# Kernel tuning notes

Hardware: AMD Instinct MI355X
Metric: run time of the kernel (lower is better)

## Reference

```python
import jax, jax.numpy as jnp
import numpy as np

RADIUS = 0.25
N_SAMPLE = 4096
N_NEIGHBOR = 32
OFF = 512   # voxel-coordinate offset so hashed coords are non-negative
M = 1024    # per-axis range of the voxel hash


def _bin_map():
    # 3^3 = 27 neighbor voxel offsets in {-1,0,1}^3 (Point2Voxel.extract_bin for D=3)
    g = np.stack(np.meshgrid(*([[-1, 0, 1]] * 3), indexing='ij'), -1).reshape(-1, 3)
    return jnp.asarray(g, dtype=jnp.int32)


def _hash(k):
    # k: [..., 3] int32 voxel coords -> unique int32 key (fits: 1024^3 < 2^31)
    return ((k[..., 0] + OFF) * M + (k[..., 1] + OFF)) * M + (k[..., 2] + OFF)


def setup_inputs() -> dict:
    key = jax.random.key(0)
    k1, k2 = jax.random.split(key)
    pos = jax.random.normal(k1, (8, 100000, 3), jnp.float32)
    feat = jax.random.normal(k2, (8, 100000, 64), jnp.float32)
    return {"pos": pos, "feat": feat}


def _graph_one(pos_b, rk):
    """Voxel-hash based neighbor sampling for one point cloud [N,3]."""
    N = pos_b.shape[0]
    vox = jnp.floor(pos_b / RADIUS).astype(jnp.int32)          # [N,3] voxel keys
    hkeys = _hash(vox)                                          # [N]
    order = jnp.argsort(hkeys)                                  # sort points by voxel (hash table)
    skeys = hkeys[order]
    kc, kn = jax.random.split(rk)
    centers = jax.random.randint(kc, (N_SAMPLE,), 0, N)         # sampled center point ids
    nk = _hash(vox[centers][:, None, :] + _bin_map()[None])     # [S,27] neighbor voxel keys
    lo = jnp.searchsorted(skeys, nk, side='left')               # bucket start  [S,27]
    hi = jnp.searchsorted(skeys, nk, side='right')              # bucket end    [S,27]
    counts = hi - lo                                            # bucket sizes
    cum = jnp.cumsum(counts, axis=1)                            # [S,27]
    total = cum[:, -1]                                          # candidates per center (>=1)
    # sample N_NEIGHBOR candidate slots uniformly over all neighbor-voxel points
    r = jax.random.randint(kn, (N_SAMPLE, N_NEIGHBOR), 0, 1 << 30) % total[:, None]
    slot = (r[:, :, None] >= cum[:, None, :]).sum(-1)           # which of the 27 voxels
    cum_ex = jnp.concatenate([jnp.zeros_like(cum[:, :1]), cum[:, :-1]], axis=1)
    prev = jnp.take_along_axis(cum_ex, slot, axis=1)
    start = jnp.take_along_axis(lo, slot, axis=1)
    src = order[start + (r - prev)]                             # [S,K] source point ids
    return centers, src


def reference(pos, feat):
    B, N, D = pos.shape
    C = feat.shape[-1]
    rks = jax.random.split(jax.random.key(42), B)
    centers, src = jax.vmap(_graph_one)(pos, rks)               # [B,S], [B,S,K]
    bidx = jnp.arange(B)[:, None]
    center_flag = jnp.zeros((B, N), pos.dtype).at[bidx, centers].set(1.0)
    src_flag = jnp.zeros((B, N), pos.dtype).at[bidx, src.reshape(B, -1)].set(1.0)
    b3 = jnp.arange(B)[:, None, None]
    pos_src = pos[b3, src]                                      # [B,S,K,3] gather
    pos_ctr = pos[bidx, centers]                                # [B,S,3]
    rel = pos_src - pos_ctr[:, :, None, :]                      # edge geometry
    f_src = feat[b3, src]                                       # [B,S,K,C] gather
    out = jnp.concatenate([rel, f_src], axis=-1)                # [B,S,K,3+C]
    return out, src, centers, center_flag, src_flag
```

## Files before the change

kernel.cpp:

```cpp
#include <hip/hip_runtime.h>
#include <stdint.h>

#define NB 8
#define NPTS 100000
#define NS 4096
#define NN 32
#define NCH 64
#define CLG 18
#define CELLS (1 << CLG)
#define CMASK (CELLS - 1)

#define OUT_MAIN 0ull
#define OUT_SRC  70254592ull
#define OUT_CTR  71303168ull
#define OUT_CF   71335936ull
#define OUT_SF   72135936ull

typedef float f32x4 __attribute__((ext_vector_type(4)));

__host__ __device__ static inline uint32_t rotl32(uint32_t v, int d) {
    return (v << d) | (v >> (32 - d));
}

__host__ __device__ static inline void tf2x32(uint32_t k0, uint32_t k1,
                                              uint32_t x0, uint32_t x1,
                                              uint32_t& o0, uint32_t& o1) {
    uint32_t ks2 = k0 ^ k1 ^ 0x1BD11BDAu;
    x0 += k0; x1 += k1;
    x0 += x1; x1 = rotl32(x1, 13); x1 ^= x0;
    x0 += x1; x1 = rotl32(x1, 15); x1 ^= x0;
    x0 += x1; x1 = rotl32(x1, 26); x1 ^= x0;
    x0 += x1; x1 = rotl32(x1, 6);  x1 ^= x0;
    x0 += k1; x1 += ks2 + 1u;
    x0 += x1; x1 = rotl32(x1, 17); x1 ^= x0;
    x0 += x1; x1 = rotl32(x1, 29); x1 ^= x0;
    x0 += x1; x1 = rotl32(x1, 16); x1 ^= x0;
    x0 += x1; x1 = rotl32(x1, 24); x1 ^= x0;
    x0 += ks2; x1 += k0 + 2u;
    x0 += x1; x1 = rotl32(x1, 13); x1 ^= x0;
    x0 += x1; x1 = rotl32(x1, 15); x1 ^= x0;
    x0 += x1; x1 = rotl32(x1, 26); x1 ^= x0;
    x0 += x1; x1 = rotl32(x1, 6);  x1 ^= x0;
    x0 += k0; x1 += k1 + 3u;
    x0 += x1; x1 = rotl32(x1, 17); x1 ^= x0;
    x0 += x1; x1 = rotl32(x1, 29); x1 ^= x0;
    x0 += x1; x1 = rotl32(x1, 16); x1 ^= x0;
    x0 += x1; x1 = rotl32(x1, 24); x1 ^= x0;
    x0 += k1; x1 += ks2 + 4u;
    x0 += x1; x1 = rotl32(x1, 13); x1 ^= x0;
    x0 += x1; x1 = rotl32(x1, 15); x1 ^= x0;
    x0 += x1; x1 = rotl32(x1, 26); x1 ^= x0;
    x0 += x1; x1 = rotl32(x1, 6);  x1 ^= x0;
    x0 += ks2; x1 += k0 + 5u;
    o0 = x0; o1 = x1;
}

struct RngKeys {
    uint32_t c0[NB], c1[NB];
    uint32_t n0[NB], n1[NB];
};

__device__ static inline uint32_t pbits32(uint32_t k0, uint32_t k1, uint32_t u) {
    uint32_t o0, o1;
    tf2x32(k0, k1, 0u, u, o0, o1);
    return o0 ^ o1;
}

__device__ static inline int cellidx(const float* __restrict__ p) {
    int vx = ((int)floorf(p[0] * 4.0f) + 32) & 63;
    int vy = ((int)floorf(p[1] * 4.0f) + 32) & 63;
    int vz = ((int)floorf(p[2] * 4.0f) + 32) & 63;
    return vx | (vy << 6) | (vz << 12);
}

__global__ void k_zero(int* __restrict__ cnt, int* __restrict__ bctr,
                       float4* __restrict__ flags4) {
    int t = blockIdx.x * blockDim.x + threadIdx.x;
    cnt[t] = 0;
    if (t < (2 * NB * NPTS) / 4) flags4[t] = make_float4(0.f, 0.f, 0.f, 0.f);
    if (t < NB) bctr[t] = 0;
}

__global__ void k_count(const float* __restrict__ pos, int* __restrict__ cnt,
                        int* __restrict__ cidxOf) {
    int t = blockIdx.x * blockDim.x + threadIdx.x;
    int b = t / NPTS;
    int cidx = cellidx(pos + (size_t)t * 3);
    cidxOf[t] = cidx;
    atomicAdd(&cnt[((size_t)b << CLG) + cidx], 1);
}

__global__ void k_starts(const int* __restrict__ cnt, int* __restrict__ cursor,
                         int* __restrict__ bctr) {
    __shared__ int sdata[256];
    __shared__ int sbase;
    int t = blockIdx.x * blockDim.x + threadIdx.x;
    int tid = threadIdx.x;
    int b = t >> CLG;
    int c = cnt[t];
    sdata[tid] = c;
    __syncthreads();
    for (int off = 1; off < 256; off <<= 1) {
        int x = (tid >= off) ? sdata[tid - off] : 0;
        __syncthreads();
        sdata[tid] += x;
        __syncthreads();
    }
    if (tid == 255) sbase = atomicAdd(&bctr[b], sdata[255]);
    __syncthreads();
    cursor[t] = sbase + sdata[tid] - c;
}

__global__ void k_scatter(const int* __restrict__ cidxOf, int* __restrict__ cursor,
                          int* __restrict__ listA) {
    int t = blockIdx.x * blockDim.x + threadIdx.x;
    int b = t / NPTS, i = t - b * NPTS;
    size_t gc = ((size_t)b << CLG) + cidxOf[t];
    int a = atomicAdd(&cursor[gc], 1);
    listA[(size_t)b * NPTS + a] = i;
}

__global__ void k_rank(const int* __restrict__ cidxOf, const int* __restrict__ cnt,
                       const int* __restrict__ cursor,
                       const int* __restrict__ listA, int* __restrict__ listB) {
    int t = blockIdx.x * blockDim.x + threadIdx.x;
    int b = t / NPTS, i = t - b * NPTS;
    size_t gc = ((size_t)b << CLG) + cidxOf[t];
    int c = cnt[gc];
    int s0 = cursor[gc] - c;
    const int* L = listA + (size_t)b * NPTS + s0;
    int rank = 0;
    for (int k = 0; k < c; k++) rank += (L[k] < i) ? 1 : 0;
    listB[(size_t)b * NPTS + s0 + rank] = i;
}

__global__ void k_sel(RngKeys keys, const int* __restrict__ cidxOf,
                      const int* __restrict__ cnt, const int* __restrict__ cursor,
                      const int* __restrict__ listB,
                      int* __restrict__ centers_ws, int* __restrict__ src_ws,
                      float* __restrict__ out_ctr, float* __restrict__ out_cf,
                      float* __restrict__ out_src, float* __restrict__ out_sf) {
    __shared__ int scnt[8][27];
    __shared__ int slo[8][27];
    int tid = threadIdx.x;
    int g = tid >> 5, n = tid & 31;
    int bs = blockIdx.x * 8 + g;
    int b = bs >> 12, s = bs & (NS - 1);
    uint32_t lower_c = pbits32(keys.c0[b], keys.c1[b], (uint32_t)s);
    int c = (int)(lower_c % 100000u);
    int ccell = cidxOf[(size_t)b * NPTS + c];
    if (n < 27) {
        int ncell = (ccell + (n / 9 - 1) + ((n / 3) % 3 - 1) * 64
                           + (n % 3 - 1) * 4096) & CMASK;
        size_t gc = ((size_t)b << CLG) + ncell;
        int cc = cnt[gc];
        scnt[g][n] = cc;
        slo[g][n] = cursor[gc] - cc;
    }
    if (n == 0) {
        centers_ws[bs] = c;
        out_ctr[bs] = (float)c;
        out_cf[(size_t)b * NPTS + c] = 1.0f;
    }
    __syncthreads();
    uint32_t lower = pbits32(keys.n0[b], keys.n1[b], (uint32_t)(s * NN + n));
    int total = 0;
    #pragma unroll
    for (int i = 0; i < 27; i++) total += scnt[g][i];
    int r = (int)(lower & 0x3FFFFFFFu) % total;
    int slot = 0, prev = 0, acc = 0;
    #pragma unroll
    for (int i = 0; i < 27; i++) {
        acc += scnt[g][i];
        if (r >= acc) { slot = i + 1; prev = acc; }
    }
    int pos_in = slo[g][slot] + (r - prev);
    int src = listB[(size_t)b * NPTS + pos_in];
    int oi = bs * NN + n;
    src_ws[oi] = src;
    out_src[oi] = (float)src;
    out_sf[(size_t)b * NPTS + src] = 1.0f;
}

__global__ void k_gather(const float* __restrict__ pos, const float* __restrict__ feat,
                         const int* __restrict__ centers_ws, const int* __restrict__ src_ws,
                         float* __restrict__ out) {
    __shared__ float sbuf[64 * 67];
    int t = threadIdx.x;
    long long row0 = (long long)blockIdx.x * 64;
    int g0 = t >> 4,          q0 = t & 15;
    int g1 = (t + 512) >> 4,  q1 = t & 15;
    long long rowA = row0 + g0, rowB = row0 + g1;
    int bA = (int)(rowA >> 17), bB = (int)(rowB >> 17);
    int srcA = src_ws[rowA];
    int srcB = src_ws[rowB];
    const float4 fvA = *(const float4*)(feat + ((size_t)bA * NPTS + srcA) * NCH + 4 * q0);
    const float4 fvB = *(const float4*)(feat + ((size_t)bB * NPTS + srcB) * NCH + 4 * q1);
    float* sbA = sbuf + g0 * 67;
    sbA[3 + 4 * q0 + 0] = fvA.x;
    sbA[3 + 4 * q0 + 1] = fvA.y;
    sbA[3 + 4 * q0 + 2] = fvA.z;
    sbA[3 + 4 * q0 + 3] = fvA.w;
    float* sbB = sbuf + g1 * 67;
    sbB[3 + 4 * q1 + 0] = fvB.x;
    sbB[3 + 4 * q1 + 1] = fvB.y;
    sbB[3 + 4 * q1 + 2] = fvB.z;
    sbB[3 + 4 * q1 + 3] = fvB.w;
    if (t < 192) {
        int g = t / 3, q = t - g * 3;
        long long row = row0 + g;
        int b = (int)(row >> 17);
        int u = (int)(row & (NS * NN - 1));
        int s = u >> 5;
        int src = src_ws[row];
        int ctr = centers_ws[b * NS + s];
        sbuf[g * 67 + q] = pos[((size_t)b * NPTS + src) * 3 + q]
                         - pos[((size_t)b * NPTS + ctr) * 3 + q];
    }
    __syncthreads();
    f32x4* ob = (f32x4*)(out + (size_t)row0 * 67);
    const f32x4* sv = (const f32x4*)sbuf;
    __builtin_nontemporal_store(sv[t], &ob[t]);
    __builtin_nontemporal_store(sv[t + 512], &ob[t + 512]);
    if (t < 48) __builtin_nontemporal_store(sv[t + 1024], &ob[t + 1024]);
}

extern "C" void kernel_launch(void* const* d_in, const int* in_sizes, int n_in,
                              void* d_out, int out_size, void* d_ws, size_t ws_size,
                              hipStream_t stream) {
    (void)in_sizes; (void)n_in; (void)out_size; (void)ws_size;
    const float* pos = (const float*)d_in[0];
    const float* feat = (const float*)d_in[1];
    float* out = (float*)d_out;

    RngKeys keys;
    for (int b = 0; b < NB; b++) {
        uint32_t rk0, rk1, kc0, kc1, kn0, kn1;
        tf2x32(0u, 42u, 0u, (uint32_t)b, rk0, rk1);
        tf2x32(rk0, rk1, 0u, 0u, kc0, kc1);
        tf2x32(rk0, rk1, 0u, 1u, kn0, kn1);
        tf2x32(kc0, kc1, 0u, 1u, keys.c0[b], keys.c1[b]);
        tf2x32(kn0, kn1, 0u, 1u, keys.n0[b], keys.n1[b]);
    }

    int* cnt        = (int*)d_ws;
    int* cursor     = cnt + (size_t)NB * CELLS;
    int* bctr       = cursor + (size_t)NB * CELLS;
    int* cidxOf     = bctr + NB;
    int* listA      = cidxOf + (size_t)NB * NPTS;
    int* listB      = listA + (size_t)NB * NPTS;
    int* centers_ws = listB + (size_t)NB * NPTS;
    int* src_ws     = centers_ws + (size_t)NB * NS;

    k_zero   <<<(NB * CELLS) / 256, 256, 0, stream>>>(cnt, bctr,
                                                      (float4*)(out + OUT_CF));
    k_count  <<<(NB * NPTS) / 256, 256, 0, stream>>>(pos, cnt, cidxOf);
    k_starts <<<(NB * CELLS) / 256, 256, 0, stream>>>(cnt, cursor, bctr);
    k_scatter<<<(NB * NPTS) / 256, 256, 0, stream>>>(cidxOf, cursor, listA);
    k_rank   <<<(NB * NPTS) / 256, 256, 0, stream>>>(cidxOf, cnt, cursor, listA, listB);
    k_sel    <<<(NB * NS) / 8, 256, 0, stream>>>(keys, cidxOf, cnt, cursor, listB,
                                                 centers_ws, src_ws,
                                                 out + OUT_CTR, out + OUT_CF,
                                                 out + OUT_SRC, out + OUT_SF);
    k_gather <<<(NB * NS * NN) / 64, 512, 0, stream>>>(pos, feat, centers_ws, src_ws, out);
}
```

Before: 372.9 us.

## Fuse all pipeline stages into one cooperative persistent kernel with grid syncs

```diff
diff --git a/kernel.cpp b/kernel.cpp
--- a/kernel.cpp
+++ b/kernel.cpp
@@ -1,5 +1,8 @@
 #include <hip/hip_runtime.h>
+#include <hip/hip_cooperative_groups.h>
 #include <stdint.h>
+
+namespace cg = cooperative_groups;
 
 #define NB 8
 #define NPTS 100000
@@ -9,6 +12,9 @@
 #define CLG 18
 #define CELLS (1 << CLG)
 #define CMASK (CELLS - 1)
+#define NBLK 512
+#define NTHR 512
+#define GSIZE (NBLK * NTHR)
 
 #define OUT_MAIN 0ull
 #define OUT_SRC  70254592ull
@@ -71,6 +77,175 @@
     int vy = ((int)floorf(p[1] * 4.0f) + 32) & 63;
     int vz = ((int)floorf(p[2] * 4.0f) + 32) & 63;
     return vx | (vy << 6) | (vz << 12);
+}
+
+struct Args {
+    const float* pos; const float* feat; float* out;
+    int* cnt; int* cursor; int* bctr; int* cidxOf;
+    int* listA; int* listB; int* centers_ws; int* src_ws;
+    RngKeys keys;
+};
+
+__global__ __launch_bounds__(NTHR, 4) void k_mega(Args a) {
+    __shared__ int smem[4352];
+    __shared__ int sbase;
+    cg::grid_group grid = cg::this_grid();
+    int tid = threadIdx.x, bid = blockIdx.x;
+    int gt = bid * NTHR + tid;
+
+    for (int t = gt; t < (NB * CELLS) / 4; t += GSIZE)
+        ((int4*)a.cnt)[t] = make_int4(0, 0, 0, 0);
+    float* flags = a.out + OUT_CF;
+    for (int t = gt; t < (2 * NB * NPTS) / 4; t += GSIZE)
+        ((float4*)flags)[t] = make_float4(0.f, 0.f, 0.f, 0.f);
+    if (gt < NB) a.bctr[gt] = 0;
+    grid.sync();
+
+    for (int t = gt; t < NB * NPTS; t += GSIZE) {
+        int b = t / NPTS;
+        int cidx = cellidx(a.pos + (size_t)t * 3);
+        a.cidxOf[t] = cidx;
+        atomicAdd(&a.cnt[((size_t)b << CLG) + cidx], 1);
+    }
+    grid.sync();
+
+    for (int chunk = 0; chunk < 2; ++chunk) {
+        int base_cell = (chunk * NBLK + bid) * 2048;
+        int b = base_cell >> CLG;
+        int4 c4 = ((const int4*)a.cnt)[(base_cell >> 2) + tid];
+        int s1 = c4.x + c4.y, s2 = s1 + c4.z, s3 = s2 + c4.w;
+        smem[tid] = s3;
+        __syncthreads();
+        for (int off = 1; off < 512; off <<= 1) {
+            int x = (tid >= off) ? smem[tid - off] : 0;
+            __syncthreads();
+            smem[tid] += x;
+            __syncthreads();
+        }
+        int incl = smem[tid];
+        if (tid == 511) sbase = atomicAdd(&a.bctr[b], smem[511]);
+        __syncthreads();
+        int base = sbase + incl - s3;
+        int4 cur;
+        cur.x = base;
+        cur.y = base + c4.x;
+        cur.z = base + s1;
+        cur.w = base + s2;
+        ((int4*)a.cursor)[(base_cell >> 2) + tid] = cur;
+        __syncthreads();
+    }
+    grid.sync();
+
+    for (int t = gt; t < NB * NPTS; t += GSIZE) {
+        int b = t / NPTS, i = t - b * NPTS;
+        size_t gc = ((size_t)b << CLG) + a.cidxOf[t];
+        int p = atomicAdd(&a.cursor[gc], 1);
+        a.listA[(size_t)b * NPTS + p] = i;
+    }
+    grid.sync();
+
+    for (int t = gt; t < NB * NPTS; t += GSIZE) {
+        int b = t / NPTS, i = t - b * NPTS;
+        size_t gc = ((size_t)b << CLG) + a.cidxOf[t];
+        int c = a.cnt[gc];
+        int s0 = a.cursor[gc] - c;
+        const int* L = a.listA + (size_t)b * NPTS + s0;
+        int rank = 0;
+        for (int k = 0; k < c; k++) rank += (L[k] < i) ? 1 : 0;
+        a.listB[(size_t)b * NPTS + s0 + rank] = i;
+    }
+    grid.sync();
+
+    {
+        int (*scnt)[27] = (int(*)[27])smem;
+        int (*slo)[27]  = (int(*)[27])(smem + 16 * 27);
+        int g = tid >> 5, n = tid & 31;
+        for (int it = 0; it < 4; ++it) {
+            int bs = (it * NBLK + bid) * 16 + g;
+            int b = bs >> 12, s = bs & (NS - 1);
+            uint32_t lower_c = pbits32(a.keys.c0[b], a.keys.c1[b], (uint32_t)s);
+            int c = (int)(lower_c % 100000u);
+            int ccell = a.cidxOf[(size_t)b * NPTS + c];
+            __syncthreads();
+            if (n < 27) {
+                int ncell = (ccell + (n / 9 - 1) + ((n / 3) % 3 - 1) * 64
+                                   + (n % 3 - 1) * 4096) & CMASK;
+                size_t gc = ((size_t)b << CLG) + ncell;
+                int cc = a.cnt[gc];
+                scnt[g][n] = cc;
+                slo[g][n] = a.cursor[gc] - cc;
+            }
+            if (n == 0) {
+                a.centers_ws[bs] = c;
+                a.out[OUT_CTR + bs] = (float)c;
+                a.out[OUT_CF + (size_t)b * NPTS + c] = 1.0f;
+            }
+            __syncthreads();
+            uint32_t lower = pbits32(a.keys.n0[b], a.keys.n1[b],
+                                     (uint32_t)(s * NN + n));
+            int total = 0;
+            #pragma unroll
+            for (int i = 0; i < 27; i++) total += scnt[g][i];
+            int r = (int)(lower & 0x3FFFFFFFu) % total;
+            int slot = 0, prev = 0, acc = 0;
+            #pragma unroll
+            for (int i = 0; i < 27; i++) {
+                acc += scnt[g][i];
+                if (r >= acc) { slot = i + 1; prev = acc; }
+            }
+            int pos_in = slo[g][slot] + (r - prev);
+            int src = a.listB[(size_t)b * NPTS + pos_in];
+            int oi = bs * NN + n;
+            a.src_ws[oi] = src;
+            a.out[OUT_SRC + oi] = (float)src;
+            a.out[OUT_SF + (size_t)b * NPTS + src] = 1.0f;
+        }
+    }
+    grid.sync();
+
+    {
+        float* sbuf = (float*)smem;
+        for (int it = 0; it < 32; ++it) {
+            long long tile = (long long)it * NBLK + bid;
+            long long row0 = tile * 64;
+            int g0 = tid >> 4, q0 = tid & 15;
+            int g1 = g0 + 32;
+            long long rowA = row0 + g0, rowB = row0 + g1;
+            int bA = (int)(rowA >> 17), bB = (int)(rowB >> 17);
+            int srcA = a.src_ws[rowA];
+            int srcB = a.src_ws[rowB];
+            const float4 fvA = *(const float4*)(a.feat + ((size_t)bA * NPTS + srcA) * NCH + 4 * q0);
+            const float4 fvB = *(const float4*)(a.feat + ((size_t)bB * NPTS + srcB) * NCH + 4 * q0);
+            __syncthreads();
+            float* sbA = sbuf + g0 * 67;
+            sbA[3 + 4 * q0 + 0] = fvA.x;
+            sbA[3 + 4 * q0 + 1] = fvA.y;
+            sbA[3 + 4 * q0 + 2] = fvA.z;
+            sbA[3 + 4 * q0 + 3] = fvA.w;
+            float* sbB = sbuf + g1 * 67;
+            sbB[3 + 4 * q0 + 0] = fvB.x;
+            sbB[3 + 4 * q0 + 1] = fvB.y;
+            sbB[3 + 4 * q0 + 2] = fvB.z;
+            sbB[3 + 4 * q0 + 3] = fvB.w;
+            if (tid < 192) {
+                int g = tid / 3, q = tid - g * 3;
+                long long row = row0 + g;
+                int b = (int)(row >> 17);
+                int u = (int)(row & (NS * NN - 1));
+                int s = u >> 5;
+                int src = a.src_ws[row];
+                int ctr = a.centers_ws[b * NS + s];
+                sbuf[g * 67 + q] = a.pos[((size_t)b * NPTS + src) * 3 + q]
+                                 - a.pos[((size_t)b * NPTS + ctr) * 3 + q];
+            }
+            __syncthreads();
+            f32x4* ob = (f32x4*)(a.out + (size_t)row0 * 67);
+            const f32x4* sv = (const f32x4*)sbuf;
+            __builtin_nontemporal_store(sv[tid], &ob[tid]);
+            __builtin_nontemporal_store(sv[tid + 512], &ob[tid + 512]);
+            if (tid < 48) __builtin_nontemporal_store(sv[tid + 1024], &ob[tid + 1024]);
+        }
+    }
 }
 
 __global__ void k_zero(int* __restrict__ cnt, int* __restrict__ bctr,
@@ -252,15 +427,28 @@
     int* centers_ws = listB + (size_t)NB * NPTS;
     int* src_ws     = centers_ws + (size_t)NB * NS;
 
-    k_zero   <<<(NB * CELLS) / 256, 256, 0, stream>>>(cnt, bctr,
-                                                      (float4*)(out + OUT_CF));
-    k_count  <<<(NB * NPTS) / 256, 256, 0, stream>>>(pos, cnt, cidxOf);
-    k_starts <<<(NB * CELLS) / 256, 256, 0, stream>>>(cnt, cursor, bctr);
-    k_scatter<<<(NB * NPTS) / 256, 256, 0, stream>>>(cidxOf, cursor, listA);
-    k_rank   <<<(NB * NPTS) / 256, 256, 0, stream>>>(cidxOf, cnt, cursor, listA, listB);
-    k_sel    <<<(NB * NS) / 8, 256, 0, stream>>>(keys, cidxOf, cnt, cursor, listB,
-                                                 centers_ws, src_ws,
-                                                 out + OUT_CTR, out + OUT_CF,
-                                                 out + OUT_SRC, out + OUT_SF);
-    k_gather <<<(NB * NS * NN) / 64, 512, 0, stream>>>(pos, feat, centers_ws, src_ws, out);
-}
+    Args args;
+    args.pos = pos; args.feat = feat; args.out = out;
+    args.cnt = cnt; args.cursor = cursor; args.bctr = bctr; args.cidxOf = cidxOf;
+    args.listA = listA; args.listB = listB;
+    args.centers_ws = centers_ws; args.src_ws = src_ws;
+    args.keys = keys;
+
+    void* kparams[] = { &args };
+    hipError_t err = hipLaunchCooperativeKernel((const void*)k_mega, dim3(NBLK),
+                                                dim3(NTHR), kparams, 0, stream);
+    if (err != hipSuccess) {
+        k_zero   <<<(NB * CELLS) / 256, 256, 0, stream>>>(cnt, bctr,
+                                                          (float4*)(out + OUT_CF));
+        k_count  <<<(NB * NPTS) / 256, 256, 0, stream>>>(pos, cnt, cidxOf);
+        k_starts <<<(NB * CELLS) / 256, 256, 0, stream>>>(cnt, cursor, bctr);
+        k_scatter<<<(NB * NPTS) / 256, 256, 0, stream>>>(cidxOf, cursor, listA);
+        k_rank   <<<(NB * NPTS) / 256, 256, 0, stream>>>(cidxOf, cnt, cursor, listA, listB);
+        k_sel    <<<(NB * NS) / 8, 256, 0, stream>>>(keys, cidxOf, cnt, cursor, listB,
+                                                     centers_ws, src_ws,
+                                                     out + OUT_CTR, out + OUT_CF,
+                                                     out + OUT_SRC, out + OUT_SF);
+        k_gather <<<(NB * NS * NN) / 64, 512, 0, stream>>>(pos, feat, centers_ws,
+                                                           src_ws, out);
+    }
+}
```

New measurement: 690.3 us. 1.85x slower.

## Fuse neighbor selection with feature gather and vectorize workspace zeroing

Applied to the files above, without the earlier changes.

```diff
diff --git a/kernel.cpp b/kernel.cpp
--- a/kernel.cpp
+++ b/kernel.cpp
@@ -73,10 +73,10 @@
     return vx | (vy << 6) | (vz << 12);
 }
 
-__global__ void k_zero(int* __restrict__ cnt, int* __restrict__ bctr,
+__global__ void k_zero(int4* __restrict__ cnt4, int* __restrict__ bctr,
                        float4* __restrict__ flags4) {
     int t = blockIdx.x * blockDim.x + threadIdx.x;
-    cnt[t] = 0;
+    cnt4[t] = make_int4(0, 0, 0, 0);
     if (t < (2 * NB * NPTS) / 4) flags4[t] = make_float4(0.f, 0.f, 0.f, 0.f);
     if (t < NB) bctr[t] = 0;
 }
@@ -134,14 +134,16 @@
     listB[(size_t)b * NPTS + s0 + rank] = i;
 }
 
-__global__ void k_sel(RngKeys keys, const int* __restrict__ cidxOf,
-                      const int* __restrict__ cnt, const int* __restrict__ cursor,
-                      const int* __restrict__ listB,
-                      int* __restrict__ centers_ws, int* __restrict__ src_ws,
-                      float* __restrict__ out_ctr, float* __restrict__ out_cf,
-                      float* __restrict__ out_src, float* __restrict__ out_sf) {
+__global__ __launch_bounds__(256) void k_selgather(
+        RngKeys keys, const float* __restrict__ pos, const float* __restrict__ feat,
+        const int* __restrict__ cidxOf, const int* __restrict__ cnt,
+        const int* __restrict__ cursor, const int* __restrict__ listB,
+        float* __restrict__ out) {
     __shared__ int scnt[8][27];
     __shared__ int slo[8][27];
+    __shared__ int ssrc[256];
+    __shared__ float sctr[8][3];
+    __shared__ float sbuf[64 * 67];
     int tid = threadIdx.x;
     int g = tid >> 5, n = tid & 31;
     int bs = blockIdx.x * 8 + g;
@@ -157,10 +159,10 @@
         scnt[g][n] = cc;
         slo[g][n] = cursor[gc] - cc;
     }
+    if (n < 3) sctr[g][n] = pos[((size_t)b * NPTS + c) * 3 + n];
     if (n == 0) {
-        centers_ws[bs] = c;
-        out_ctr[bs] = (float)c;
-        out_cf[(size_t)b * NPTS + c] = 1.0f;
+        out[OUT_CTR + bs] = (float)c;
+        out[OUT_CF + (size_t)b * NPTS + c] = 1.0f;
     }
     __syncthreads();
     uint32_t lower = pbits32(keys.n0[b], keys.n1[b], (uint32_t)(s * NN + n));
@@ -176,53 +178,40 @@
     }
     int pos_in = slo[g][slot] + (r - prev);
     int src = listB[(size_t)b * NPTS + pos_in];
-    int oi = bs * NN + n;
-    src_ws[oi] = src;
-    out_src[oi] = (float)src;
-    out_sf[(size_t)b * NPTS + src] = 1.0f;
-}
-
-__global__ void k_gather(const float* __restrict__ pos, const float* __restrict__ feat,
-                         const int* __restrict__ centers_ws, const int* __restrict__ src_ws,
-                         float* __restrict__ out) {
-    __shared__ float sbuf[64 * 67];
-    int t = threadIdx.x;
-    long long row0 = (long long)blockIdx.x * 64;
-    int g0 = t >> 4,          q0 = t & 15;
-    int g1 = (t + 512) >> 4,  q1 = t & 15;
-    long long rowA = row0 + g0, rowB = row0 + g1;
-    int bA = (int)(rowA >> 17), bB = (int)(rowB >> 17);
-    int srcA = src_ws[rowA];
-    int srcB = src_ws[rowB];
-    const float4 fvA = *(const float4*)(feat + ((size_t)bA * NPTS + srcA) * NCH + 4 * q0);
-    const float4 fvB = *(const float4*)(feat + ((size_t)bB * NPTS + srcB) * NCH + 4 * q1);
-    float* sbA = sbuf + g0 * 67;
-    sbA[3 + 4 * q0 + 0] = fvA.x;
-    sbA[3 + 4 * q0 + 1] = fvA.y;
-    sbA[3 + 4 * q0 + 2] = fvA.z;
-    sbA[3 + 4 * q0 + 3] = fvA.w;
-    float* sbB = sbuf + g1 * 67;
-    sbB[3 + 4 * q1 + 0] = fvB.x;
-    sbB[3 + 4 * q1 + 1] = fvB.y;
-    sbB[3 + 4 * q1 + 2] = fvB.z;
-    sbB[3 + 4 * q1 + 3] = fvB.w;
-    if (t < 192) {
-        int g = t / 3, q = t - g * 3;
-        long long row = row0 + g;
-        int b = (int)(row >> 17);
-        int u = (int)(row & (NS * NN - 1));
-        int s = u >> 5;
-        int src = src_ws[row];
-        int ctr = centers_ws[b * NS + s];
-        sbuf[g * 67 + q] = pos[((size_t)b * NPTS + src) * 3 + q]
-                         - pos[((size_t)b * NPTS + ctr) * 3 + q];
-    }
-    __syncthreads();
-    f32x4* ob = (f32x4*)(out + (size_t)row0 * 67);
-    const f32x4* sv = (const f32x4*)sbuf;
-    __builtin_nontemporal_store(sv[t], &ob[t]);
-    __builtin_nontemporal_store(sv[t + 512], &ob[t + 512]);
-    if (t < 48) __builtin_nontemporal_store(sv[t + 1024], &ob[t + 1024]);
+    ssrc[tid] = src;
+    out[OUT_SRC + (size_t)bs * NN + n] = (float)src;
+    out[OUT_SF + (size_t)b * NPTS + src] = 1.0f;
+    size_t outbase = (size_t)blockIdx.x * 256 * 67;
+    for (int j = 0; j < 4; ++j) {
+        __syncthreads();
+        int rloc = tid >> 2, q = tid & 3;
+        int src_r = ssrc[j * 64 + rloc];
+        const float* f = feat + ((size_t)b * NPTS + src_r) * NCH + q * 16;
+        float4 f0 = *(const float4*)(f + 0);
+        float4 f1 = *(const float4*)(f + 4);
+        float4 f2 = *(const float4*)(f + 8);
+        float4 f3 = *(const float4*)(f + 12);
+        float* sb = sbuf + rloc * 67 + 3 + q * 16;
+        sb[0] = f0.x;  sb[1] = f0.y;  sb[2] = f0.z;  sb[3] = f0.w;
+        sb[4] = f1.x;  sb[5] = f1.y;  sb[6] = f1.z;  sb[7] = f1.w;
+        sb[8] = f2.x;  sb[9] = f2.y;  sb[10] = f2.z; sb[11] = f2.w;
+        sb[12] = f3.x; sb[13] = f3.y; sb[14] = f3.z; sb[15] = f3.w;
+        if (tid < 192) {
+            int gr = tid / 3, qq = tid - gr * 3;
+            int R2 = j * 64 + gr;
+            int s2 = ssrc[R2];
+            sbuf[gr * 67 + qq] = pos[((size_t)b * NPTS + s2) * 3 + qq]
+                               - sctr[R2 >> 5][qq];
+        }
+        __syncthreads();
+        f32x4* ob = (f32x4*)(out + outbase + (size_t)j * 64 * 67);
+        const f32x4* sv = (const f32x4*)sbuf;
+        __builtin_nontemporal_store(sv[tid], &ob[tid]);
+        __builtin_nontemporal_store(sv[tid + 256], &ob[tid + 256]);
+        __builtin_nontemporal_store(sv[tid + 512], &ob[tid + 512]);
+        __builtin_nontemporal_store(sv[tid + 768], &ob[tid + 768]);
+        if (tid < 48) __builtin_nontemporal_store(sv[tid + 1024], &ob[tid + 1024]);
+    }
 }
 
 extern "C" void kernel_launch(void* const* d_in, const int* in_sizes, int n_in,
@@ -249,18 +238,13 @@
     int* cidxOf     = bctr + NB;
     int* listA      = cidxOf + (size_t)NB * NPTS;
     int* listB      = listA + (size_t)NB * NPTS;
-    int* centers_ws = listB + (size_t)NB * NPTS;
-    int* src_ws     = centers_ws + (size_t)NB * NS;
-
-    k_zero   <<<(NB * CELLS) / 256, 256, 0, stream>>>(cnt, bctr,
-                                                      (float4*)(out + OUT_CF));
-    k_count  <<<(NB * NPTS) / 256, 256, 0, stream>>>(pos, cnt, cidxOf);
-    k_starts <<<(NB * CELLS) / 256, 256, 0, stream>>>(cnt, cursor, bctr);
-    k_scatter<<<(NB * NPTS) / 256, 256, 0, stream>>>(cidxOf, cursor, listA);
-    k_rank   <<<(NB * NPTS) / 256, 256, 0, stream>>>(cidxOf, cnt, cursor, listA, listB);
-    k_sel    <<<(NB * NS) / 8, 256, 0, stream>>>(keys, cidxOf, cnt, cursor, listB,
-                                                 centers_ws, src_ws,
-                                                 out + OUT_CTR, out + OUT_CF,
-                                                 out + OUT_SRC, out + OUT_SF);
-    k_gather <<<(NB * NS * NN) / 64, 512, 0, stream>>>(pos, feat, centers_ws, src_ws, out);
-}
+
+    k_zero     <<<(NB * CELLS / 4) / 256, 256, 0, stream>>>((int4*)cnt, bctr,
+                                                            (float4*)(out + OUT_CF));
+    k_count    <<<(NB * NPTS) / 256, 256, 0, stream>>>(pos, cnt, cidxOf);
+    k_starts   <<<(NB * CELLS) / 256, 256, 0, stream>>>(cnt, cursor, bctr);
+    k_scatter  <<<(NB * NPTS) / 256, 256, 0, stream>>>(cidxOf, cursor, listA);
+    k_rank     <<<(NB * NPTS) / 256, 256, 0, stream>>>(cidxOf, cnt, cursor, listA, listB);
+    k_selgather<<<(NB * NS) / 8, 256, 0, stream>>>(keys, pos, feat, cidxOf, cnt,
+                                                   cursor, listB, out);
+}
```

New measurement: 378.4 us. No clear change (+1.5%).
